# Optimization experiments

Measured on AMD Instinct MI355X. Metric: run time of the kernel, lower is better.

## Reference

```python
import jax, jax.numpy as jnp
import numpy as np

B, IN_DIM, OUT_DIM, MV = 8192, 256, 256, 8


def setup_inputs() -> dict:
    key = jax.random.key(0)
    k1, k2 = jax.random.split(key)
    x = jax.random.normal(k1, (B, IN_DIM, MV), dtype=jnp.float32)
    weights = jax.random.normal(k2, (IN_DIM, OUT_DIM, MV), dtype=jnp.float32) * 0.01
    bias = jnp.zeros((OUT_DIM, MV), dtype=jnp.float32)
    return {"x": x, "weights": weights, "bias": bias}


def reference(x, weights, bias):
    # Simplified GA-3D geometric product, summed over in_dim (j), per out_dim (i):
    #   y[..., i, 0] = sum_j x[..., j, 0]*W[j,i,0] + x[..., j, 1]*W[j,i,1] + x[..., j, 2]*W[j,i,2]
    #   y[..., i, 4] = sum_j x[..., j, 1]*W[j,i,2] - x[..., j, 2]*W[j,i,1] + x[..., j, 4]*W[j,i,0]
    #   all other multivector components receive only the bias.
    # Scalar component: dot over first 3 multivector slots.
    c0 = jnp.einsum('bjk,jik->bi', x[..., 0:3], weights[..., 0:3])  # (B, OUT_DIM)
    # Bivector component e23: x1*w2 - x2*w1 + x4*w0.
    xv = jnp.stack([x[..., 1], -x[..., 2], x[..., 4]], axis=-1)          # (B, IN_DIM, 3)
    wv = jnp.stack([weights[..., 2], weights[..., 1], weights[..., 0]], axis=-1)  # (IN_DIM, OUT_DIM, 3)
    c4 = jnp.einsum('bjk,jik->bi', xv, wv)  # (B, OUT_DIM)
    y = jnp.broadcast_to(bias, (x.shape[0],) + bias.shape)  # (B, OUT_DIM, MV)
    y = y.at[..., 0].add(c0).at[..., 4].add(c4)
    return y
```

## Files before the change

### kernel.cpp

```cpp
#include <hip/hip_runtime.h>
#include <hip/hip_bf16.h>

typedef __attribute__((ext_vector_type(4))) float f32x4;
typedef __attribute__((ext_vector_type(4))) unsigned int u32x4;
typedef __attribute__((ext_vector_type(8))) short bf16x8;

__device__ __forceinline__ short f2bf(float f) {
  __hip_bfloat16 h = __float2bfloat16(f);
  return __builtin_bit_cast(short, h);
}

__global__ __launch_bounds__(256) void ga_prep_B(const float* __restrict__ W,
                                                 short* __restrict__ Bp) {
  const int gid = blockIdx.x * 256 + threadIdx.x;
  const int l  = gid & 63;
  const int cg = (gid >> 6) & 15;
  const int it = gid >> 10;
  const int ln = l & 15, q = l >> 4;
  const int i  = cg * 16 + ln;
  const int j0 = it * 8 + q * 2;
  const float4* W4 = (const float4*)W;

  bf16x8 o;
#pragma unroll
  for (int jj = 0; jj < 2; ++jj) {
    const float4 wv = W4[((j0 + jj) * 256 + i) * 2];
    o[jj * 4 + 0] = f2bf(wv.x); o[jj * 4 + 1] = f2bf(wv.y);
    o[jj * 4 + 2] = f2bf(wv.z); o[jj * 4 + 3] = 0;
  }
  *(bf16x8*)&Bp[(size_t)gid * 8] = o;
}

__global__ __launch_bounds__(256) void ga_prep_A(const float* __restrict__ x,
                                                 short* __restrict__ A) {
  const int g = blockIdx.x * 256 + threadIdx.x;
  const float4* xp = (const float4*)x + (size_t)g * 4;
  const float4 a0 = xp[0], a1 = xp[1], b0 = xp[2], b1 = xp[3];
  bf16x8 o;
  o[0] = f2bf(a0.x); o[1] = f2bf(a0.y); o[2] = f2bf(a0.z); o[3] = f2bf(a1.x);
  o[4] = f2bf(b0.x); o[5] = f2bf(b0.y); o[6] = f2bf(b0.z); o[7] = f2bf(b1.x);
  *(bf16x8*)&A[(size_t)g * 8] = o;
}

__global__ __launch_bounds__(256, 6) void ga_gemm(
    const short* __restrict__ A, const short* __restrict__ Bp,
    const float* __restrict__ bias, float* __restrict__ y) {
  const int t = threadIdx.x, lane = t & 63, w = t >> 6;
  const int ln = lane & 15, qq = lane >> 4;
  const int bm = blockIdx.x >> 2, cb = blockIdx.x & 3;
  const int R0 = bm * 16, cg = cb * 4 + w;
  const int i = cg * 16 + ln;

  const short* ap = A + (size_t)(R0 + ln) * 1024 + qq * 8;
  const short* bp = Bp + (size_t)cg * 512 + lane * 8;

  bf16x8 Af[4], Bf[4];
#define LA(it, b) { Af[b] = *(const bf16x8*)(ap + (it) * 32); }
#define LB(it, b) { Bf[b] = *(const bf16x8*)(bp + (size_t)(it) * 8192); }
  LA(0, 0) LA(1, 1) LA(2, 2) LA(3, 3)
  LB(0, 0) LB(1, 1) LB(2, 2) LB(3, 3)

  f32x4 acc0 = {}, acc1 = {};
#pragma unroll
  for (int it = 0; it < 32; ++it) {
    const bf16x8 af = Af[it & 3];
    const bf16x8 F = Bf[it & 3];
    const u32x4 fu = __builtin_bit_cast(u32x4, F);
    u32x4 gu;
    gu.x = fu.y << 16;
    gu.y = ((fu.x >> 16) | (fu.x << 16)) ^ 0x8000u;
    gu.z = fu.w << 16;
    gu.w = ((fu.z >> 16) | (fu.z << 16)) ^ 0x8000u;
    const bf16x8 G = __builtin_bit_cast(bf16x8, gu);
    acc0 = __builtin_amdgcn_mfma_f32_16x16x32_bf16(af, F, acc0, 0, 0, 0);
    acc1 = __builtin_amdgcn_mfma_f32_16x16x32_bf16(af, G, acc1, 0, 0, 0);
    if (it + 4 < 32) { LA(it + 4, it & 3) LB(it + 4, it & 3) }
  }

  const f32x4 bv0 = ((const f32x4*)bias)[i * 2];
  const f32x4 bv1 = ((const f32x4*)bias)[i * 2 + 1];
  f32x4* yp = (f32x4*)y + ((size_t)(R0 + qq * 4) * 256 + i) * 2;
#pragma unroll
  for (int r = 0; r < 4; ++r) {
    f32x4 o0 = bv0, o1 = bv1;
    o0[0] += acc0[r];
    o1[0] += acc1[r];
    __builtin_nontemporal_store(o0, yp + (size_t)r * 512);
    __builtin_nontemporal_store(o1, yp + (size_t)r * 512 + 1);
  }
}

extern "C" void kernel_launch(void* const* d_in, const int* in_sizes, int n_in,
                              void* d_out, int out_size, void* d_ws, size_t ws_size,
                              hipStream_t stream) {
  const float* x = (const float*)d_in[0];
  const float* W = (const float*)d_in[1];
  const float* bias = (const float*)d_in[2];
  float* y = (float*)d_out;
  short* Bp = (short*)d_ws;
  short* A = (short*)d_ws + (1 << 18);

  ga_prep_B<<<dim3(128), dim3(256), 0, stream>>>(W, Bp);
  ga_prep_A<<<dim3(4096), dim3(256), 0, stream>>>(x, A);
  ga_gemm<<<dim3(2048), dim3(256), 0, stream>>>(A, Bp, bias, y);
}
```

Before: 154.2 us.

## Hand-schedule GEMM loads with inline asm waitcnts and swizzle block order

```diff
diff --git a/kernel.cpp b/kernel.cpp
--- a/kernel.cpp
+++ b/kernel.cpp
@@ -9,6 +9,12 @@
   __hip_bfloat16 h = __float2bfloat16(f);
   return __builtin_bit_cast(short, h);
 }
+
+#define WAITV(N)                                            \
+  {                                                         \
+    asm volatile("s_waitcnt vmcnt(" #N ")" ::: "memory");   \
+    __builtin_amdgcn_sched_barrier(0);                      \
+  }
 
 __global__ __launch_bounds__(256) void ga_prep_B(const float* __restrict__ W,
                                                  short* __restrict__ Bp) {
@@ -42,40 +48,66 @@
   *(bf16x8*)&A[(size_t)g * 8] = o;
 }
 
-__global__ __launch_bounds__(256, 6) void ga_gemm(
+__global__ __launch_bounds__(256, 4) void ga_gemm(
     const short* __restrict__ A, const short* __restrict__ Bp,
     const float* __restrict__ bias, float* __restrict__ y) {
   const int t = threadIdx.x, lane = t & 63, w = t >> 6;
   const int ln = lane & 15, qq = lane >> 4;
-  const int bm = blockIdx.x >> 2, cb = blockIdx.x & 3;
+  const int bid = blockIdx.x;
+  const int bm = (bid & 7) | ((bid >> 5) << 3);
+  const int cb = (bid >> 3) & 3;
   const int R0 = bm * 16, cg = cb * 4 + w;
   const int i = cg * 16 + ln;
 
-  const short* ap = A + (size_t)(R0 + ln) * 1024 + qq * 8;
-  const short* bp = Bp + (size_t)cg * 512 + lane * 8;
+  const short* apL = A + (size_t)(R0 + ln) * 1024 + qq * 8;
+  const short* bpL = Bp + (size_t)cg * 512 + lane * 8;
 
   bf16x8 Af[4], Bf[4];
-#define LA(it, b) { Af[b] = *(const bf16x8*)(ap + (it) * 32); }
-#define LB(it, b) { Bf[b] = *(const bf16x8*)(bp + (size_t)(it) * 8192); }
-  LA(0, 0) LA(1, 1) LA(2, 2) LA(3, 3)
-  LB(0, 0) LB(1, 1) LB(2, 2) LB(3, 3)
+
+#define GLA(slot, IMM)                                               \
+  asm volatile("global_load_dwordx4 %0, %1, off offset:" #IMM        \
+               : "=&v"(Af[slot])                                     \
+               : "v"(apL)                                            \
+               : "memory");
+#define GLB(slot)                                                    \
+  {                                                                  \
+    asm volatile("global_load_dwordx4 %0, %1, off"                   \
+                 : "=&v"(Bf[slot])                                   \
+                 : "v"(bpL)                                          \
+                 : "memory");                                        \
+    bpL += 8192;                        \
+  }
+#define PAIR(slot, IMM) { GLA(slot, IMM) GLB(slot) }
+
+  PAIR(0, 0) PAIR(1, 64) PAIR(2, 128) PAIR(3, 192)
 
   f32x4 acc0 = {}, acc1 = {};
-#pragma unroll
-  for (int it = 0; it < 32; ++it) {
-    const bf16x8 af = Af[it & 3];
-    const bf16x8 F = Bf[it & 3];
-    const u32x4 fu = __builtin_bit_cast(u32x4, F);
-    u32x4 gu;
-    gu.x = fu.y << 16;
-    gu.y = ((fu.x >> 16) | (fu.x << 16)) ^ 0x8000u;
-    gu.z = fu.w << 16;
-    gu.w = ((fu.z >> 16) | (fu.z << 16)) ^ 0x8000u;
-    const bf16x8 G = __builtin_bit_cast(bf16x8, gu);
-    acc0 = __builtin_amdgcn_mfma_f32_16x16x32_bf16(af, F, acc0, 0, 0, 0);
-    acc1 = __builtin_amdgcn_mfma_f32_16x16x32_bf16(af, G, acc1, 0, 0, 0);
-    if (it + 4 < 32) { LA(it + 4, it & 3) LB(it + 4, it & 3) }
+
+#define ITER(it, N, IMM)                                                      \
+  {                                                                           \
+    WAITV(N);                                                                 \
+    const bf16x8 af = Af[(it) & 3];                                           \
+    const bf16x8 F = Bf[(it) & 3];                                            \
+    const u32x4 fu = __builtin_bit_cast(u32x4, F);                            \
+    u32x4 gu;                                                                 \
+    gu.x = fu.y << 16;                                         \
+    gu.y = ((fu.x >> 16) | (fu.x << 16)) ^ 0x8000u;            \
+    gu.z = fu.w << 16;                                                        \
+    gu.w = ((fu.z >> 16) | (fu.z << 16)) ^ 0x8000u;                           \
+    const bf16x8 G = __builtin_bit_cast(bf16x8, gu);                          \
+    acc0 = __builtin_amdgcn_mfma_f32_16x16x32_bf16(af, F, acc0, 0, 0, 0);     \
+    acc1 = __builtin_amdgcn_mfma_f32_16x16x32_bf16(af, G, acc1, 0, 0, 0);     \
+    if ((it) + 4 < 32) PAIR((it) & 3, IMM)                                    \
   }
+
+  ITER(0, 6, 256)   ITER(1, 6, 320)   ITER(2, 6, 384)   ITER(3, 6, 448)
+  ITER(4, 6, 512)   ITER(5, 6, 576)   ITER(6, 6, 640)   ITER(7, 6, 704)
+  ITER(8, 6, 768)   ITER(9, 6, 832)   ITER(10, 6, 896)  ITER(11, 6, 960)
+  ITER(12, 6, 1024) ITER(13, 6, 1088) ITER(14, 6, 1152) ITER(15, 6, 1216)
+  ITER(16, 6, 1280) ITER(17, 6, 1344) ITER(18, 6, 1408) ITER(19, 6, 1472)
+  ITER(20, 6, 1536) ITER(21, 6, 1600) ITER(22, 6, 1664) ITER(23, 6, 1728)
+  ITER(24, 6, 1792) ITER(25, 6, 1856) ITER(26, 6, 1920) ITER(27, 6, 1984)
+  ITER(28, 6, 0)    ITER(29, 4, 0)    ITER(30, 2, 0)    ITER(31, 0, 0)
 
   const f32x4 bv0 = ((const f32x4*)bias)[i * 2];
   const f32x4 bv1 = ((const f32x4*)bias)[i * 2 + 1];
```

Measured after the change: 155.0 us. Within noise of the previous version (+0.5%).
